# Optimization experiments

Hardware: AMD Instinct MI355X
Metric: run time of the kernel (lower is better)

The kernel has to match this reference:

```python
import jax, jax.numpy as jnp
import numpy as np

N = 50000      # nodes
E = 800000     # edges
H = 4          # attention heads
C = 64         # per-head channels (channel_in = channel_out = 64)
DIN = 128      # raw node feature dim (lazy Linear infers this)
D1 = H * C     # 256 = channel_in*4 concat dim
EPS = 1e-16    # PyG softmax eps
LN_EPS = 1e-5


def setup_inputs() -> dict:
    key = jax.random.key(0)
    ks = jax.random.split(key, 20)
    p = lambda k, shape: jax.random.normal(k, shape, jnp.float32) * 0.05
    return {
        "x": jax.random.normal(ks[0], (N, DIN), jnp.float32),
        "edge_index": jax.random.randint(ks[1], (2, E), 0, N, jnp.int32),
        # conv1 (GATConv with separate src/dst transforms, bipartite lazy mode)
        "Wsrc1": p(ks[2], (DIN, D1)), "Wdst1": p(ks[3], (DIN, D1)),
        "atts1": p(ks[4], (H, C)), "attd1": p(ks[5], (H, C)), "b1": p(ks[6], (D1,)),
        # lin1 skip
        "Wlin1": p(ks[7], (DIN, D1)), "blin1": p(ks[8], (D1,)),
        # LayerNorm
        "gamma": jnp.ones((D1,), jnp.float32), "beta": jnp.zeros((D1,), jnp.float32),
        # conv2
        "Wsrc2": p(ks[9], (D1, D1)), "Wdst2": p(ks[10], (D1, D1)),
        "atts2": p(ks[11], (H, C)), "attd2": p(ks[12], (H, C)), "b2": p(ks[13], (D1,)),
        # lin2 skip
        "Wlin2": p(ks[14], (D1, D1)), "blin2": p(ks[15], (D1,)),
    }


def gat_conv(x, src, dst, Wsrc, Wdst, atts, attd, bias):
    """PyG GATConv: gather -> leaky_relu score -> segment softmax over dst -> scatter-add."""
    n = x.shape[0]
    xs = (x @ Wsrc).reshape(n, H, C)   # source-side transform
    xd = (x @ Wdst).reshape(n, H, C)   # destination-side transform
    a_s = jnp.sum(xs * atts, axis=-1)  # [N,H]
    a_d = jnp.sum(xd * attd, axis=-1)  # [N,H]
    e = jax.nn.leaky_relu(a_s[src] + a_d[dst], 0.2)          # [E,H]
    m = jax.ops.segment_max(e, dst, num_segments=n)           # [N,H]
    m = jnp.where(jnp.isfinite(m), m, 0.0)                    # nodes with no in-edges
    ex = jnp.exp(e - m[dst])
    den = jax.ops.segment_sum(ex, dst, num_segments=n)
    alpha = ex / (den[dst] + EPS)                             # [E,H]
    out = jax.ops.segment_sum(xs[src] * alpha[:, :, None], dst, num_segments=n)
    return out.reshape(n, H * C) + bias                       # concat heads + bias


def reference(x, edge_index, Wsrc1, Wdst1, atts1, attd1, b1, Wlin1, blin1,
              gamma, beta, Wsrc2, Wdst2, atts2, attd2, b2, Wlin2, blin2):
    src, dst = edge_index[0], edge_index[1]
    h = gat_conv(x, src, dst, Wsrc1, Wdst1, atts1, attd1, b1) + x @ Wlin1 + blin1
    mu = jnp.mean(h, axis=-1, keepdims=True)
    var = jnp.mean((h - mu) ** 2, axis=-1, keepdims=True)
    h = (h - mu) * jax.lax.rsqrt(var + LN_EPS) * gamma + beta
    h = jax.nn.relu(h)
    out = gat_conv(h, src, dst, Wsrc2, Wdst2, atts2, attd2, b2) + h @ Wlin2 + blin2
    return out
```

## Files before the change

kernel.cpp:

```cpp
#include <hip/hip_runtime.h>
#include <float.h>

constexpr int DIN = 128;
constexpr int D1  = 256;
constexpr int HH  = 4;
constexpr int CC  = 64;

typedef _Float16 f16;
typedef __attribute__((ext_vector_type(2))) _Float16 f16x2;
typedef __attribute__((ext_vector_type(4))) _Float16 f16x4;
typedef __attribute__((ext_vector_type(8))) _Float16 f16x8;
typedef __attribute__((ext_vector_type(2))) float f32x2;
typedef __attribute__((ext_vector_type(4))) float f32x4;
typedef unsigned char u8;

#if __has_builtin(__builtin_amdgcn_cvt_pk_f32_fp8) && __has_builtin(__builtin_amdgcn_cvt_pk_fp8_f32)
#define HAS_CVT_FP8 1
#else
#define HAS_CVT_FP8 0
#include <hip/hip_fp8.h>
#endif

__device__ __forceinline__ u8 f2fp8(float f) {
#if HAS_CVT_FP8
    return (u8)(__builtin_amdgcn_cvt_pk_fp8_f32(f, f, 0, false) & 0xff);
#else
    __hip_fp8_e4m3 t(f);
    return (u8)t.__x;
#endif
}

__device__ __forceinline__ void fp8fma(unsigned w, float a, float4& acc) {
#if HAS_CVT_FP8
    f32x2 lo = __builtin_amdgcn_cvt_pk_f32_fp8((int)w, false);
    f32x2 hi = __builtin_amdgcn_cvt_pk_f32_fp8((int)w, true);
    acc.x = fmaf(lo[0], a, acc.x);
    acc.y = fmaf(lo[1], a, acc.y);
    acc.z = fmaf(hi[0], a, acc.z);
    acc.w = fmaf(hi[1], a, acc.w);
#else
    __hip_fp8_e4m3 b0, b1, b2, b3;
    b0.__x = (w) & 0xff; b1.__x = (w >> 8) & 0xff;
    b2.__x = (w >> 16) & 0xff; b3.__x = (w >> 24) & 0xff;
    acc.x = fmaf((float)b0, a, acc.x);
    acc.y = fmaf((float)b1, a, acc.y);
    acc.z = fmaf((float)b2, a, acc.z);
    acc.w = fmaf((float)b3, a, acc.w);
#endif
}

__device__ __forceinline__ float wave_sum(float v) {
    #pragma unroll
    for (int off = 32; off > 0; off >>= 1) v += __shfl_down(v, off, 64);
    return v;
}

__global__ __launch_bounds__(256) void pack_w_all_kernel(
        const float* __restrict__ Wsrc1, const float* __restrict__ Wlin1,
        const float* __restrict__ Wsrc2, const float* __restrict__ Wlin2,
        f16* __restrict__ WpS1, f16* __restrict__ WpL1,
        f16* __restrict__ WpS2, f16* __restrict__ WpL2) {
    int idx = blockIdx.x * 256 + threadIdx.x;
    const float *Wa, *Wb;
    f16 *Wpa, *Wpb;
    if (idx < DIN * D1) { Wa = Wsrc1; Wb = Wlin1; Wpa = WpS1; Wpb = WpL1; }
    else {
        idx -= DIN * D1;
        if (idx >= D1 * D1) return;
        Wa = Wsrc2; Wb = Wlin2; Wpa = WpS2; Wpb = WpL2;
    }
    int j    = idx & 7;
    int lane = (idx >> 3) & 63;
    int t    = idx >> 9;
    int ct   = t & 15, kt = t >> 4;
    int k    = kt * 32 + (lane >> 4) * 8 + j;
    int col  = ct * 16 + (lane & 15);
    size_t widx = (size_t)k * D1 + col;
    Wpa[idx] = (f16)Wa[widx];
    Wpb[idx] = (f16)Wb[widx];
}

__global__ __launch_bounds__(512) void make_v_all_kernel(
        const float* __restrict__ Wsrc1, const float* __restrict__ Wdst1,
        const float* __restrict__ atts1, const float* __restrict__ attd1,
        const float* __restrict__ Wsrc2, const float* __restrict__ Wdst2,
        const float* __restrict__ atts2, const float* __restrict__ attd2,
        float* __restrict__ Vs1, float* __restrict__ Vd1,
        float* __restrict__ Vs2, float* __restrict__ Vd2) {
    int kb = blockIdx.x;
    int w = threadIdx.x >> 6, lane = threadIdx.x & 63;
    int mat = w >> 2, h = w & 3;
    const float *W, *att;
    float* V;
    int k;
    if (kb < DIN) {
        k = kb;
        W = mat ? Wdst1 : Wsrc1; att = mat ? attd1 : atts1; V = mat ? Vd1 : Vs1;
    } else {
        k = kb - DIN;
        W = mat ? Wdst2 : Wsrc2; att = mat ? attd2 : atts2; V = mat ? Vd2 : Vs2;
    }
    float v = W[(size_t)k * D1 + h * CC + lane] * att[h * CC + lane];
    v = wave_sum(v);
    if (lane == 0) V[k * HH + h] = v;
}

__global__ __launch_bounds__(256) void cvt_scores_kernel(
        const float* __restrict__ X, const float* __restrict__ Vs,
        const float* __restrict__ Vd, f16* __restrict__ X16,
        float* __restrict__ a_s, float* __restrict__ a_d, int n) {
    constexpr int K = DIN, C = 32, SH = 5;
    __shared__ float4 VsL[K + 4];
    __shared__ float4 VdL[K + 4];
    for (int k = threadIdx.x; k < K; k += 256) {
        int ki = k + (k >> SH);
        VsL[ki] = reinterpret_cast<const float4*>(Vs)[k];
        VdL[ki] = reinterpret_cast<const float4*>(Vd)[k];
    }
    __syncthreads();

    const int lane  = threadIdx.x & 63;
    const int wid   = threadIdx.x >> 6;
    const int node  = blockIdx.x * 64 + wid * 16 + (lane >> 2);
    const int chunk = lane & 3;
    const int nodec = min(node, n - 1);
    const float* xp = X + (size_t)nodec * K + chunk * C;

    float xv[C];
    #pragma unroll
    for (int b = 0; b < C / 4; ++b) {
        float4 v = reinterpret_cast<const float4*>(xp)[b];
        xv[b * 4 + 0] = v.x; xv[b * 4 + 1] = v.y;
        xv[b * 4 + 2] = v.z; xv[b * 4 + 3] = v.w;
    }
    if (node < n) {
        f16* op = X16 + (size_t)node * K + chunk * C;
        #pragma unroll
        for (int b = 0; b < C / 8; ++b) {
            f16x8 o;
            #pragma unroll
            for (int t = 0; t < 8; ++t) o[t] = (f16)xv[b * 8 + t];
            reinterpret_cast<f16x8*>(op)[b] = o;
        }
    }

    float ps0 = 0.f, ps1 = 0.f, ps2 = 0.f, ps3 = 0.f;
    float pd0 = 0.f, pd1 = 0.f, pd2 = 0.f, pd3 = 0.f;
    #pragma unroll
    for (int t = 0; t < C; ++t) {
        int k  = chunk * C + t;
        int ki = k + (k >> SH);
        float xf = xv[t];
        float4 vs = VsL[ki];
        float4 vd = VdL[ki];
        ps0 = fmaf(xf, vs.x, ps0); ps1 = fmaf(xf, vs.y, ps1);
        ps2 = fmaf(xf, vs.z, ps2); ps3 = fmaf(xf, vs.w, ps3);
        pd0 = fmaf(xf, vd.x, pd0); pd1 = fmaf(xf, vd.y, pd1);
        pd2 = fmaf(xf, vd.z, pd2); pd3 = fmaf(xf, vd.w, pd3);
    }
    #pragma unroll
    for (int off = 1; off <= 2; off <<= 1) {
        ps0 += __shfl_xor(ps0, off, 64); ps1 += __shfl_xor(ps1, off, 64);
        ps2 += __shfl_xor(ps2, off, 64); ps3 += __shfl_xor(ps3, off, 64);
        pd0 += __shfl_xor(pd0, off, 64); pd1 += __shfl_xor(pd1, off, 64);
        pd2 += __shfl_xor(pd2, off, 64); pd3 += __shfl_xor(pd3, off, 64);
    }
    if (node < n) {
        float psv = chunk == 0 ? ps0 : chunk == 1 ? ps1 : chunk == 2 ? ps2 : ps3;
        float pdv = chunk == 0 ? pd0 : chunk == 1 ? pd1 : chunk == 2 ? pd2 : pd3;
        a_s[node * 4 + chunk] = psv;
        a_d[node * 4 + chunk] = pdv;
    }
}

__global__ __launch_bounds__(256) void deg_kernel(
        const int* __restrict__ dst, int* __restrict__ deg, int ne) {
    int e = blockIdx.x * 256 + threadIdx.x;
    if (e < ne) atomicAdd(deg + dst[e], 1);
}

__global__ __launch_bounds__(1024) void scan_phase1(
        const int* __restrict__ deg, int* __restrict__ partial,
        int* __restrict__ blocksum, int n) {
    __shared__ int tmp[1024];
    const int tid = threadIdx.x;
    int i = blockIdx.x * 1024 + tid;
    int v = (i < n) ? deg[i] : 0;
    tmp[tid] = v;
    __syncthreads();
    #pragma unroll
    for (int off = 1; off < 1024; off <<= 1) {
        int t = (tid >= off) ? tmp[tid - off] : 0;
        __syncthreads();
        tmp[tid] += t;
        __syncthreads();
    }
    if (i < n) partial[i] = tmp[tid];
    if (tid == 1023) blocksum[blockIdx.x] = tmp[1023];
}

__global__ __launch_bounds__(64) void scan_phase2(int* __restrict__ bs, int nb) {
    int lane = threadIdx.x;
    if (nb <= 64) {
        int v = (lane < nb) ? bs[lane] : 0;
        #pragma unroll
        for (int off = 1; off < 64; off <<= 1) {
            int t = __shfl_up(v, off, 64);
            if (lane >= off) v += t;
        }
        if (lane < nb) bs[lane] = v;
    } else if (lane == 0) {
        int acc = 0;
        for (int i = 0; i < nb; ++i) { acc += bs[i]; bs[i] = acc; }
    }
}

__global__ __launch_bounds__(1024) void scan_phase3(
        const int* __restrict__ partial, const int* __restrict__ bs,
        const int* __restrict__ deg, int* __restrict__ rowptr,
        int* __restrict__ degcur, int n) {
    int i = blockIdx.x * 1024 + threadIdx.x;
    if (i >= n) return;
    int add  = blockIdx.x ? bs[blockIdx.x - 1] : 0;
    int incl = partial[i] + add;
    rowptr[i + 1] = incl;
    degcur[i] = incl - deg[i];
    if (i == 0) rowptr[0] = 0;
}

__global__ __launch_bounds__(256) void fill_kernel(
        const int* __restrict__ src, const int* __restrict__ dst,
        int* __restrict__ cursor, int* __restrict__ srcs_csr, int ne) {
    int e = blockIdx.x * 256 + threadIdx.x;
    if (e >= ne) return;
    int pos = atomicAdd(cursor + dst[e], 1);
    srcs_csr[pos] = src[e];
}

template <int K>
__global__ __launch_bounds__(256) void gemm_dual_mfma(
        const f16* __restrict__ A, const f16* __restrict__ Wp1,
        const f16* __restrict__ Wp2, const float* __restrict__ bias1,
        const float* __restrict__ bias2, u8* __restrict__ O1,
        f16* __restrict__ O2, int n) {
    constexpr int KT = K / 32;
    const int lane = threadIdx.x & 63;
    const int w    = threadIdx.x >> 6;
    const int row0 = blockIdx.x * 64;
    const int col0 = w * 64;

    f32x4 acc1[4][4], acc2[4][4];
    const f32x4 zero = {0.f, 0.f, 0.f, 0.f};
    #pragma unroll
    for (int i = 0; i < 4; ++i)
        #pragma unroll
        for (int j = 0; j < 4; ++j) { acc1[i][j] = zero; acc2[i][j] = zero; }

    const f16* Arow[4];
    #pragma unroll
    for (int rf = 0; rf < 4; ++rf) {
        int ar = min(row0 + rf * 16 + (lane & 15), n - 1);
        Arow[rf] = A + (size_t)ar * K + (lane >> 4) * 8;
    }
    const f16* Wb1 = Wp1 + ((size_t)(w * 4) * 64 + lane) * 8;
    const f16* Wb2 = Wp2 + ((size_t)(w * 4) * 64 + lane) * 8;

    #pragma unroll
    for (int kt = 0; kt < KT; ++kt) {
        f16x8 a[4];
        #pragma unroll
        for (int rf = 0; rf < 4; ++rf)
            a[rf] = *reinterpret_cast<const f16x8*>(Arow[rf] + kt * 32);
        #pragma unroll
        for (int cf = 0; cf < 4; ++cf) {
            f16x8 b1v = *reinterpret_cast<const f16x8*>(Wb1 + (size_t)(kt * 16 + cf) * 512);
            f16x8 b2v = *reinterpret_cast<const f16x8*>(Wb2 + (size_t)(kt * 16 + cf) * 512);
            #pragma unroll
            for (int rf = 0; rf < 4; ++rf) {
                acc1[rf][cf] = __builtin_amdgcn_mfma_f32_16x16x32_f16(a[rf], b1v, acc1[rf][cf], 0, 0, 0);
                acc2[rf][cf] = __builtin_amdgcn_mfma_f32_16x16x32_f16(a[rf], b2v, acc2[rf][cf], 0, 0, 0);
            }
        }
    }

    #pragma unroll
    for (int cf = 0; cf < 4; ++cf) {
        const int col = col0 + cf * 16 + (lane & 15);
        const float bsum = bias1[col] + bias2[col];
        #pragma unroll
        for (int rf = 0; rf < 4; ++rf) {
            #pragma unroll
            for (int r = 0; r < 4; ++r) {
                const int row = row0 + rf * 16 + (lane >> 4) * 4 + r;
                if (row < n) {
                    O1[(size_t)row * D1 + col] = f2fp8(acc1[rf][cf][r]);
                    O2[(size_t)row * D1 + col] = (f16)(acc2[rf][cf][r] + bsum);
                }
            }
        }
    }
}

#define ALDS_STRIDE 66

__device__ __forceinline__ float4 gat_node_acc(
        const int* __restrict__ srcs, const float* __restrict__ a_s,
        const u8* __restrict__ xs, f16* __restrict__ alds,
        const float* __restrict__ a_d_row, int base, int deg, int lane) {
    const int h = lane >> 4;
    const int j = lane & 15;
    const float adv = a_d_row[h];
    float den = 0.f;
    float4 acc = {0.f, 0.f, 0.f, 0.f};
    const f16* arow = alds + h * ALDS_STRIDE;

    for (int c0 = 0; c0 < deg; c0 += 16) {
        const int cnt = min(16, deg - c0);
        const int idx = c0 + j;
        const bool valid = idx < deg;
        const int sl = srcs[base + min(idx, deg - 1)];
        {
            float e = a_s[(size_t)sl * 4 + h] + adv;
            e = e > 0.f ? e : 0.2f * e;
            float a = valid ? __expf(e) : 0.f;
            den += a;
            alds[h * ALDS_STRIDE + j] = (f16)a;
        }
        asm volatile("s_waitcnt lgkmcnt(0)" ::: "memory");

        const int sv = sl;
        for (int i = 0; i < cnt; i += 4) {
            int s1 = __shfl(sv, i, 64);
            int s2 = __shfl(sv, i + 1, 64);
            int s3 = __shfl(sv, i + 2, 64);
            int s4 = __shfl(sv, i + 3, 64);
            f16x2 alA = *reinterpret_cast<const f16x2*>(arow + i);
            f16x2 alB = *reinterpret_cast<const f16x2*>(arow + i + 2);
            unsigned x1 = *reinterpret_cast<const unsigned*>(xs + (size_t)s1 * D1 + lane * 4);
            unsigned x2 = *reinterpret_cast<const unsigned*>(xs + (size_t)s2 * D1 + lane * 4);
            unsigned x3 = *reinterpret_cast<const unsigned*>(xs + (size_t)s3 * D1 + lane * 4);
            unsigned x4 = *reinterpret_cast<const unsigned*>(xs + (size_t)s4 * D1 + lane * 4);
            fp8fma(x1, (float)alA.x, acc);
            fp8fma(x2, (float)alA.y, acc);
            fp8fma(x3, (float)alB.x, acc);
            fp8fma(x4, (float)alB.y, acc);
        }
    }

    #pragma unroll
    for (int off = 1; off < 16; off <<= 1)
        den += __shfl_xor(den, off, 64);
    const float invd = 1.f / (den + 1e-16f);
    acc.x *= invd; acc.y *= invd; acc.z *= invd; acc.w *= invd;
    return acc;
}

__global__ __launch_bounds__(256) void gat_gather_ln_kernel(
        const int* __restrict__ rowptr, const int* __restrict__ srcs,
        const float* __restrict__ a_s1, const float* __restrict__ a_d1,
        const u8* __restrict__ xs, const f16* __restrict__ skip,
        const float* __restrict__ gamma, const float* __restrict__ beta,
        const float* __restrict__ Vs2, const float* __restrict__ Vd2,
        f16* __restrict__ hout, float* __restrict__ a_s2,
        float* __restrict__ a_d2, int n) {
    __shared__ f16 alpha_lds[4][4 * ALDS_STRIDE];
    const int wid = threadIdx.x >> 6, lane = threadIdx.x & 63;
    const int d = blockIdx.x * 4 + wid;
    if (d >= n) return;
    const int base = rowptr[d];
    const int deg  = rowptr[d + 1] - base;

    float4 acc = {0.f, 0.f, 0.f, 0.f};
    if (deg > 0)
        acc = gat_node_acc(srcs, a_s1, xs, alpha_lds[wid],
                           a_d1 + (size_t)d * 4, base, deg, lane);

    f16x4 sk = *reinterpret_cast<const f16x4*>(skip + (size_t)d * D1 + lane * 4);
    float4 v;
    v.x = acc.x + (float)sk[0];
    v.y = acc.y + (float)sk[1];
    v.z = acc.z + (float)sk[2];
    v.w = acc.w + (float)sk[3];

    float s  = v.x + v.y + v.z + v.w;
    float sq = v.x * v.x + v.y * v.y + v.z * v.z + v.w * v.w;
    #pragma unroll
    for (int off = 32; off > 0; off >>= 1) {
        s  += __shfl_down(s, off, 64);
        sq += __shfl_down(sq, off, 64);
    }
    s  = __shfl(s, 0, 64);
    sq = __shfl(sq, 0, 64);
    float mu  = s * (1.f / 256.f);
    float var = sq * (1.f / 256.f) - mu * mu;
    float rstd = rsqrtf(var + 1e-5f);
    float4 g = *reinterpret_cast<const float4*>(gamma + lane * 4);
    float4 b = *reinterpret_cast<const float4*>(beta + lane * 4);
    f16x4 o;
    o[0] = (f16)fmaxf((v.x - mu) * rstd * g.x + b.x, 0.f);
    o[1] = (f16)fmaxf((v.y - mu) * rstd * g.y + b.y, 0.f);
    o[2] = (f16)fmaxf((v.z - mu) * rstd * g.z + b.z, 0.f);
    o[3] = (f16)fmaxf((v.w - mu) * rstd * g.w + b.w, 0.f);
    *reinterpret_cast<f16x4*>(hout + (size_t)d * D1 + lane * 4) = o;

    float of0 = (float)o[0], of1 = (float)o[1], of2 = (float)o[2], of3 = (float)o[3];
    const float4* V4s = reinterpret_cast<const float4*>(Vs2);
    const float4* V4d = reinterpret_cast<const float4*>(Vd2);
    float4 r0 = V4s[lane * 4 + 0], r1 = V4s[lane * 4 + 1];
    float4 r2 = V4s[lane * 4 + 2], r3 = V4s[lane * 4 + 3];
    float4 ps;
    ps.x = of0 * r0.x + of1 * r1.x + of2 * r2.x + of3 * r3.x;
    ps.y = of0 * r0.y + of1 * r1.y + of2 * r2.y + of3 * r3.y;
    ps.z = of0 * r0.z + of1 * r1.z + of2 * r2.z + of3 * r3.z;
    ps.w = of0 * r0.w + of1 * r1.w + of2 * r2.w + of3 * r3.w;
    r0 = V4d[lane * 4 + 0]; r1 = V4d[lane * 4 + 1];
    r2 = V4d[lane * 4 + 2]; r3 = V4d[lane * 4 + 3];
    float4 pd;
    pd.x = of0 * r0.x + of1 * r1.x + of2 * r2.x + of3 * r3.x;
    pd.y = of0 * r0.y + of1 * r1.y + of2 * r2.y + of3 * r3.y;
    pd.z = of0 * r0.z + of1 * r1.z + of2 * r2.z + of3 * r3.z;
    pd.w = of0 * r0.w + of1 * r1.w + of2 * r2.w + of3 * r3.w;
    #pragma unroll
    for (int off = 1; off < 64; off <<= 1) {
        ps.x += __shfl_xor(ps.x, off, 64); ps.y += __shfl_xor(ps.y, off, 64);
        ps.z += __shfl_xor(ps.z, off, 64); ps.w += __shfl_xor(ps.w, off, 64);
        pd.x += __shfl_xor(pd.x, off, 64); pd.y += __shfl_xor(pd.y, off, 64);
        pd.z += __shfl_xor(pd.z, off, 64); pd.w += __shfl_xor(pd.w, off, 64);
    }
    if (lane == 0) {
        *reinterpret_cast<float4*>(a_s2 + (size_t)d * 4) = ps;
        *reinterpret_cast<float4*>(a_d2 + (size_t)d * 4) = pd;
    }
}

__global__ __launch_bounds__(256) void gat_gather_out_kernel(
        const int* __restrict__ rowptr, const int* __restrict__ srcs,
        const float* __restrict__ a_s, const float* __restrict__ a_d,
        const u8* __restrict__ xs, const f16* __restrict__ skip2,
        float* __restrict__ out, int n) {
    __shared__ f16 alpha_lds[4][4 * ALDS_STRIDE];
    const int wid = threadIdx.x >> 6, lane = threadIdx.x & 63;
    const int d = blockIdx.x * 4 + wid;
    if (d >= n) return;
    const int base = rowptr[d];
    const int deg  = rowptr[d + 1] - base;
    float4 acc = {0.f, 0.f, 0.f, 0.f};
    if (deg > 0)
        acc = gat_node_acc(srcs, a_s, xs, alpha_lds[wid],
                           a_d + (size_t)d * 4, base, deg, lane);
    f16x4 sk = *reinterpret_cast<const f16x4*>(skip2 + (size_t)d * D1 + lane * 4);
    float4 ov;
    ov.x = acc.x + (float)sk[0];
    ov.y = acc.y + (float)sk[1];
    ov.z = acc.z + (float)sk[2];
    ov.w = acc.w + (float)sk[3];
    *reinterpret_cast<float4*>(out + (size_t)d * D1 + lane * 4) = ov;
}

extern "C" void kernel_launch(void* const* d_in, const int* in_sizes, int n_in,
                              void* d_out, int out_size, void* d_ws, size_t ws_size,
                              hipStream_t stream) {
    const float* x     = (const float*)d_in[0];
    const int*   ei    = (const int*)d_in[1];
    const float* Wsrc1 = (const float*)d_in[2];
    const float* Wdst1 = (const float*)d_in[3];
    const float* atts1 = (const float*)d_in[4];
    const float* attd1 = (const float*)d_in[5];
    const float* b1    = (const float*)d_in[6];
    const float* Wlin1 = (const float*)d_in[7];
    const float* blin1 = (const float*)d_in[8];
    const float* gamma = (const float*)d_in[9];
    const float* beta  = (const float*)d_in[10];
    const float* Wsrc2 = (const float*)d_in[11];
    const float* Wdst2 = (const float*)d_in[12];
    const float* atts2 = (const float*)d_in[13];
    const float* attd2 = (const float*)d_in[14];
    const float* b2    = (const float*)d_in[15];
    const float* Wlin2 = (const float*)d_in[16];
    const float* blin2 = (const float*)d_in[17];

    const int n  = in_sizes[0] / DIN;
    const int ne = in_sizes[1] / 2;
    const int* src = ei;
    const int* dst = ei + ne;

    char* w8 = (char*)d_ws;
    size_t off = 0;
    auto alloc = [&](size_t bytes) -> void* {
        void* p = w8 + off;
        off += (bytes + 255) & ~(size_t)255;
        return p;
    };
    f16*  h16    = (f16*)alloc((size_t)n * D1 * 2);
    f16*  x16    = h16;
    u8*   xs8    = (u8*)alloc((size_t)n * D1);
    f16*  skip1  = (f16*)alloc((size_t)n * D1 * 2);
    float* a_s1  = (float*)alloc((size_t)n * HH * 4);
    float* a_d1  = (float*)alloc((size_t)n * HH * 4);
    float* a_s2  = (float*)alloc((size_t)n * HH * 4);
    float* a_d2  = (float*)alloc((size_t)n * HH * 4);
    float* Vs1   = (float*)alloc((size_t)D1 * HH * 4);
    float* Vd1   = (float*)alloc((size_t)D1 * HH * 4);
    float* Vs2   = (float*)alloc((size_t)D1 * HH * 4);
    float* Vd2   = (float*)alloc((size_t)D1 * HH * 4);
    int* rowptr   = (int*)alloc(((size_t)n + 1) * 4);
    int* degbuf   = (int*)alloc((size_t)n * 4);
    int* degcur   = (int*)alloc((size_t)n * 4);
    int* partial  = (int*)alloc((size_t)n * 4);
    int* blocksum = (int*)alloc(1024 * 4);
    int* srcs_csr = (int*)alloc((size_t)ne * 4);
    f16* WpS1  = (f16*)alloc((size_t)DIN * D1 * 2);
    f16* WpL1  = (f16*)alloc((size_t)DIN * D1 * 2);
    f16* WpS2  = (f16*)alloc((size_t)D1 * D1 * 2);
    f16* WpL2  = (f16*)alloc((size_t)D1 * D1 * 2);

    float* out = (float*)d_out;

    const int nb_node4  = (n + 3) / 4;
    const int nb_node64 = (n + 63) / 64;
    const int nb_e      = (ne + 255) / 256;
    const int nb_gemm   = (n + 63) / 64;
    const int nb_scan   = (n + 1023) / 1024;
    const int nb_pack   = (DIN * D1 + D1 * D1 + 255) / 256;

    (void)hipMemsetAsync(degbuf, 0, (size_t)n * 4, stream);
    deg_kernel<<<nb_e, 256, 0, stream>>>(dst, degbuf, ne);
    scan_phase1<<<nb_scan, 1024, 0, stream>>>(degbuf, partial, blocksum, n);
    scan_phase2<<<1, 64, 0, stream>>>(blocksum, nb_scan);
    scan_phase3<<<nb_scan, 1024, 0, stream>>>(partial, blocksum, degbuf, rowptr, degcur, n);
    fill_kernel<<<nb_e, 256, 0, stream>>>(src, dst, degcur, srcs_csr, ne);
    pack_w_all_kernel<<<nb_pack, 256, 0, stream>>>(Wsrc1, Wlin1, Wsrc2, Wlin2,
                                                   WpS1, WpL1, WpS2, WpL2);
    make_v_all_kernel<<<DIN + D1, 512, 0, stream>>>(Wsrc1, Wdst1, atts1, attd1,
                                                    Wsrc2, Wdst2, atts2, attd2,
                                                    Vs1, Vd1, Vs2, Vd2);

    cvt_scores_kernel<<<nb_node64, 256, 0, stream>>>(x, Vs1, Vd1, x16, a_s1, a_d1, n);
    gemm_dual_mfma<DIN><<<nb_gemm, 256, 0, stream>>>(x16, WpS1, WpL1, b1, blin1, xs8, skip1, n);
    gat_gather_ln_kernel<<<nb_node4, 256, 0, stream>>>(rowptr, srcs_csr, a_s1, a_d1, xs8,
                                                       skip1, gamma, beta, Vs2, Vd2,
                                                       h16, a_s2, a_d2, n);

    gemm_dual_mfma<D1><<<nb_gemm, 256, 0, stream>>>(h16, WpS2, WpL2, b2, blin2, xs8, skip1, n);
    gat_gather_out_kernel<<<nb_node4, 256, 0, stream>>>(rowptr, srcs_csr, a_s2, a_d2,
                                                        xs8, skip1, out, n);
}
```

Measured before the change: 286.4 us.

## Merge prep kernels, fold scan phase2, widen fp8 gathers, cheaper score reduction

Merges the weight packing and attention-vector kernels into one launch. The separate block-sum scan kernel is removed, and each scan_phase3 block now sums the preceding block sums itself. The GAT gather loop now loads 8 fp8 bytes per lane, so each lane covers two edges in parallel across the two wave halves, and the halves are recombined with shuffles. The final per-node score reduction is replaced by a transpose-style butterfly that uses fewer shuffles. The goal is to cut launch count, gather load instructions and shuffle traffic, at the cost of extra shuffles after the gather loop. The inline scan only works when there are at most 64 scan blocks.

```diff
diff --git a/kernel.cpp b/kernel.cpp
--- a/kernel.cpp
+++ b/kernel.cpp
@@ -55,54 +55,54 @@
     return v;
 }
 
-__global__ __launch_bounds__(256) void pack_w_all_kernel(
+__global__ __launch_bounds__(256) void prep_w_kernel(
         const float* __restrict__ Wsrc1, const float* __restrict__ Wlin1,
         const float* __restrict__ Wsrc2, const float* __restrict__ Wlin2,
+        const float* __restrict__ Wdst1, const float* __restrict__ Wdst2,
+        const float* __restrict__ atts1, const float* __restrict__ attd1,
+        const float* __restrict__ atts2, const float* __restrict__ attd2,
         f16* __restrict__ WpS1, f16* __restrict__ WpL1,
-        f16* __restrict__ WpS2, f16* __restrict__ WpL2) {
-    int idx = blockIdx.x * 256 + threadIdx.x;
-    const float *Wa, *Wb;
-    f16 *Wpa, *Wpb;
-    if (idx < DIN * D1) { Wa = Wsrc1; Wb = Wlin1; Wpa = WpS1; Wpb = WpL1; }
-    else {
-        idx -= DIN * D1;
-        if (idx >= D1 * D1) return;
-        Wa = Wsrc2; Wb = Wlin2; Wpa = WpS2; Wpb = WpL2;
-    }
-    int j    = idx & 7;
-    int lane = (idx >> 3) & 63;
-    int t    = idx >> 9;
-    int ct   = t & 15, kt = t >> 4;
-    int k    = kt * 32 + (lane >> 4) * 8 + j;
-    int col  = ct * 16 + (lane & 15);
-    size_t widx = (size_t)k * D1 + col;
-    Wpa[idx] = (f16)Wa[widx];
-    Wpb[idx] = (f16)Wb[widx];
-}
-
-__global__ __launch_bounds__(512) void make_v_all_kernel(
-        const float* __restrict__ Wsrc1, const float* __restrict__ Wdst1,
-        const float* __restrict__ atts1, const float* __restrict__ attd1,
-        const float* __restrict__ Wsrc2, const float* __restrict__ Wdst2,
-        const float* __restrict__ atts2, const float* __restrict__ attd2,
+        f16* __restrict__ WpS2, f16* __restrict__ WpL2,
         float* __restrict__ Vs1, float* __restrict__ Vd1,
-        float* __restrict__ Vs2, float* __restrict__ Vd2) {
-    int kb = blockIdx.x;
-    int w = threadIdx.x >> 6, lane = threadIdx.x & 63;
-    int mat = w >> 2, h = w & 3;
-    const float *W, *att;
-    float* V;
-    int k;
-    if (kb < DIN) {
-        k = kb;
-        W = mat ? Wdst1 : Wsrc1; att = mat ? attd1 : atts1; V = mat ? Vd1 : Vs1;
+        float* __restrict__ Vs2, float* __restrict__ Vd2, int nb_pack) {
+    if ((int)blockIdx.x < nb_pack) {
+        int idx = blockIdx.x * 256 + threadIdx.x;
+        const float *Wa, *Wb;
+        f16 *Wpa, *Wpb;
+        if (idx < DIN * D1) { Wa = Wsrc1; Wb = Wlin1; Wpa = WpS1; Wpb = WpL1; }
+        else {
+            idx -= DIN * D1;
+            if (idx >= D1 * D1) return;
+            Wa = Wsrc2; Wb = Wlin2; Wpa = WpS2; Wpb = WpL2;
+        }
+        int j    = idx & 7;
+        int lane = (idx >> 3) & 63;
+        int t    = idx >> 9;
+        int ct   = t & 15, kt = t >> 4;
+        int k    = kt * 32 + (lane >> 4) * 8 + j;
+        int col  = ct * 16 + (lane & 15);
+        size_t widx = (size_t)k * D1 + col;
+        Wpa[idx] = (f16)Wa[widx];
+        Wpb[idx] = (f16)Wb[widx];
     } else {
-        k = kb - DIN;
-        W = mat ? Wdst2 : Wsrc2; att = mat ? attd2 : atts2; V = mat ? Vd2 : Vs2;
-    }
-    float v = W[(size_t)k * D1 + h * CC + lane] * att[h * CC + lane];
-    v = wave_sum(v);
-    if (lane == 0) V[k * HH + h] = v;
+        int b2  = blockIdx.x - nb_pack;
+        int mat = b2 & 1;
+        int kb  = b2 >> 1;
+        int h = threadIdx.x >> 6, lane = threadIdx.x & 63;
+        const float *W, *att;
+        float* V;
+        int k;
+        if (kb < DIN) {
+            k = kb;
+            W = mat ? Wdst1 : Wsrc1; att = mat ? attd1 : atts1; V = mat ? Vd1 : Vs1;
+        } else {
+            k = kb - DIN;
+            W = mat ? Wdst2 : Wsrc2; att = mat ? attd2 : atts2; V = mat ? Vd2 : Vs2;
+        }
+        float v = W[(size_t)k * D1 + h * CC + lane] * att[h * CC + lane];
+        v = wave_sum(v);
+        if (lane == 0) V[k * HH + h] = v;
+    }
 }
 
 __global__ __launch_bounds__(256) void cvt_scores_kernel(
@@ -199,29 +199,22 @@
     if (tid == 1023) blocksum[blockIdx.x] = tmp[1023];
 }
 
-__global__ __launch_bounds__(64) void scan_phase2(int* __restrict__ bs, int nb) {
-    int lane = threadIdx.x;
-    if (nb <= 64) {
-        int v = (lane < nb) ? bs[lane] : 0;
-        #pragma unroll
-        for (int off = 1; off < 64; off <<= 1) {
-            int t = __shfl_up(v, off, 64);
-            if (lane >= off) v += t;
-        }
-        if (lane < nb) bs[lane] = v;
-    } else if (lane == 0) {
-        int acc = 0;
-        for (int i = 0; i < nb; ++i) { acc += bs[i]; bs[i] = acc; }
-    }
-}
-
 __global__ __launch_bounds__(1024) void scan_phase3(
-        const int* __restrict__ partial, const int* __restrict__ bs,
+        const int* __restrict__ partial, const int* __restrict__ blocksum,
         const int* __restrict__ deg, int* __restrict__ rowptr,
         int* __restrict__ degcur, int n) {
+    __shared__ int add_s;
+    if (threadIdx.x < 64) {
+        int lane = threadIdx.x;
+        int v = (lane < (int)blockIdx.x) ? blocksum[lane] : 0;
+        #pragma unroll
+        for (int off = 32; off > 0; off >>= 1) v += __shfl_down(v, off, 64);
+        if (lane == 0) add_s = v;
+    }
+    __syncthreads();
+    const int add = add_s;
     int i = blockIdx.x * 1024 + threadIdx.x;
     if (i >= n) return;
-    int add  = blockIdx.x ? bs[blockIdx.x - 1] : 0;
     int incl = partial[i] + add;
     rowptr[i + 1] = incl;
     degcur[i] = incl - deg[i];
@@ -307,12 +300,15 @@
         const int* __restrict__ srcs, const float* __restrict__ a_s,
         const u8* __restrict__ xs, f16* __restrict__ alds,
         const float* __restrict__ a_d_row, int base, int deg, int lane) {
-    const int h = lane >> 4;
-    const int j = lane & 15;
+    const int h    = lane >> 4;
+    const int j    = lane & 15;
+    const int pair = lane >> 5;
+    const int ch32 = lane & 31;
+    const f16* arow_i = alds + (ch32 >> 3) * ALDS_STRIDE;
     const float adv = a_d_row[h];
     float den = 0.f;
-    float4 acc = {0.f, 0.f, 0.f, 0.f};
-    const f16* arow = alds + h * ALDS_STRIDE;
+    float4 accLo = {0.f, 0.f, 0.f, 0.f};
+    float4 accHi = {0.f, 0.f, 0.f, 0.f};
 
     for (int c0 = 0; c0 < deg; c0 += 16) {
         const int cnt = min(16, deg - c0);
@@ -330,22 +326,33 @@
 
         const int sv = sl;
         for (int i = 0; i < cnt; i += 4) {
-            int s1 = __shfl(sv, i, 64);
-            int s2 = __shfl(sv, i + 1, 64);
-            int s3 = __shfl(sv, i + 2, 64);
-            int s4 = __shfl(sv, i + 3, 64);
-            f16x2 alA = *reinterpret_cast<const f16x2*>(arow + i);
-            f16x2 alB = *reinterpret_cast<const f16x2*>(arow + i + 2);
-            unsigned x1 = *reinterpret_cast<const unsigned*>(xs + (size_t)s1 * D1 + lane * 4);
-            unsigned x2 = *reinterpret_cast<const unsigned*>(xs + (size_t)s2 * D1 + lane * 4);
-            unsigned x3 = *reinterpret_cast<const unsigned*>(xs + (size_t)s3 * D1 + lane * 4);
-            unsigned x4 = *reinterpret_cast<const unsigned*>(xs + (size_t)s4 * D1 + lane * 4);
-            fp8fma(x1, (float)alA.x, acc);
-            fp8fma(x2, (float)alA.y, acc);
-            fp8fma(x3, (float)alB.x, acc);
-            fp8fma(x4, (float)alB.y, acc);
-        }
-    }
+            int sA = __shfl(sv, i + pair, 64);
+            int sB = __shfl(sv, i + 2 + pair, 64);
+            float aA = (float)arow_i[i + pair];
+            float aB = (float)arow_i[i + 2 + pair];
+            uint2 xA = *reinterpret_cast<const uint2*>(xs + (size_t)sA * D1 + ch32 * 8);
+            uint2 xB = *reinterpret_cast<const uint2*>(xs + (size_t)sB * D1 + ch32 * 8);
+            fp8fma(xA.x, aA, accLo);
+            fp8fma(xA.y, aA, accHi);
+            fp8fma(xB.x, aB, accLo);
+            fp8fma(xB.y, aB, accHi);
+        }
+    }
+
+    accLo.x += __shfl_xor(accLo.x, 32, 64); accLo.y += __shfl_xor(accLo.y, 32, 64);
+    accLo.z += __shfl_xor(accLo.z, 32, 64); accLo.w += __shfl_xor(accLo.w, 32, 64);
+    accHi.x += __shfl_xor(accHi.x, 32, 64); accHi.y += __shfl_xor(accHi.y, 32, 64);
+    accHi.z += __shfl_xor(accHi.z, 32, 64); accHi.w += __shfl_xor(accHi.w, 32, 64);
+
+    const int srcl = lane >> 1;
+    float l0 = __shfl(accLo.x, srcl, 64), l1 = __shfl(accLo.y, srcl, 64);
+    float l2 = __shfl(accLo.z, srcl, 64), l3 = __shfl(accLo.w, srcl, 64);
+    float h0 = __shfl(accHi.x, srcl, 64), h1 = __shfl(accHi.y, srcl, 64);
+    float h2 = __shfl(accHi.z, srcl, 64), h3 = __shfl(accHi.w, srcl, 64);
+    const bool hi = (lane & 1) != 0;
+    float4 acc;
+    acc.x = hi ? h0 : l0; acc.y = hi ? h1 : l1;
+    acc.z = hi ? h2 : l2; acc.w = hi ? h3 : l3;
 
     #pragma unroll
     for (int off = 1; off < 16; off <<= 1)
@@ -408,28 +415,34 @@
     const float4* V4d = reinterpret_cast<const float4*>(Vd2);
     float4 r0 = V4s[lane * 4 + 0], r1 = V4s[lane * 4 + 1];
     float4 r2 = V4s[lane * 4 + 2], r3 = V4s[lane * 4 + 3];
-    float4 ps;
-    ps.x = of0 * r0.x + of1 * r1.x + of2 * r2.x + of3 * r3.x;
-    ps.y = of0 * r0.y + of1 * r1.y + of2 * r2.y + of3 * r3.y;
-    ps.z = of0 * r0.z + of1 * r1.z + of2 * r2.z + of3 * r3.z;
-    ps.w = of0 * r0.w + of1 * r1.w + of2 * r2.w + of3 * r3.w;
+    float v0 = of0 * r0.x + of1 * r1.x + of2 * r2.x + of3 * r3.x;
+    float v1 = of0 * r0.y + of1 * r1.y + of2 * r2.y + of3 * r3.y;
+    float v2 = of0 * r0.z + of1 * r1.z + of2 * r2.z + of3 * r3.z;
+    float v3 = of0 * r0.w + of1 * r1.w + of2 * r2.w + of3 * r3.w;
     r0 = V4d[lane * 4 + 0]; r1 = V4d[lane * 4 + 1];
     r2 = V4d[lane * 4 + 2]; r3 = V4d[lane * 4 + 3];
-    float4 pd;
-    pd.x = of0 * r0.x + of1 * r1.x + of2 * r2.x + of3 * r3.x;
-    pd.y = of0 * r0.y + of1 * r1.y + of2 * r2.y + of3 * r3.y;
-    pd.z = of0 * r0.z + of1 * r1.z + of2 * r2.z + of3 * r3.z;
-    pd.w = of0 * r0.w + of1 * r1.w + of2 * r2.w + of3 * r3.w;
-    #pragma unroll
-    for (int off = 1; off < 64; off <<= 1) {
-        ps.x += __shfl_xor(ps.x, off, 64); ps.y += __shfl_xor(ps.y, off, 64);
-        ps.z += __shfl_xor(ps.z, off, 64); ps.w += __shfl_xor(ps.w, off, 64);
-        pd.x += __shfl_xor(pd.x, off, 64); pd.y += __shfl_xor(pd.y, off, 64);
-        pd.z += __shfl_xor(pd.z, off, 64); pd.w += __shfl_xor(pd.w, off, 64);
-    }
-    if (lane == 0) {
-        *reinterpret_cast<float4*>(a_s2 + (size_t)d * 4) = ps;
-        *reinterpret_cast<float4*>(a_d2 + (size_t)d * 4) = pd;
+    float v4 = of0 * r0.x + of1 * r1.x + of2 * r2.x + of3 * r3.x;
+    float v5 = of0 * r0.y + of1 * r1.y + of2 * r2.y + of3 * r3.y;
+    float v6 = of0 * r0.z + of1 * r1.z + of2 * r2.z + of3 * r3.z;
+    float v7 = of0 * r0.w + of1 * r1.w + of2 * r2.w + of3 * r3.w;
+
+    const bool b0 = (lane & 1) != 0;
+    float w0 = (b0 ? v1 : v0) + __shfl_xor(b0 ? v0 : v1, 1, 64);
+    float w1 = (b0 ? v3 : v2) + __shfl_xor(b0 ? v2 : v3, 1, 64);
+    float w2 = (b0 ? v5 : v4) + __shfl_xor(b0 ? v4 : v5, 1, 64);
+    float w3 = (b0 ? v7 : v6) + __shfl_xor(b0 ? v6 : v7, 1, 64);
+    const bool b1 = (lane & 2) != 0;
+    float u0 = (b1 ? w1 : w0) + __shfl_xor(b1 ? w0 : w1, 2, 64);
+    float u1 = (b1 ? w3 : w2) + __shfl_xor(b1 ? w2 : w3, 2, 64);
+    const bool b2f = (lane & 4) != 0;
+    float z = (b2f ? u1 : u0) + __shfl_xor(b2f ? u0 : u1, 4, 64);
+    z += __shfl_xor(z, 8, 64);
+    z += __shfl_xor(z, 16, 64);
+    z += __shfl_xor(z, 32, 64);
+    if (lane < 8) {
+        float* outp = (lane < 4) ? (a_s2 + (size_t)d * 4 + lane)
+                                 : (a_d2 + (size_t)d * 4 + (lane - 4));
+        *outp = z;
     }
 }
 
@@ -526,14 +539,12 @@
     (void)hipMemsetAsync(degbuf, 0, (size_t)n * 4, stream);
     deg_kernel<<<nb_e, 256, 0, stream>>>(dst, degbuf, ne);
     scan_phase1<<<nb_scan, 1024, 0, stream>>>(degbuf, partial, blocksum, n);
-    scan_phase2<<<1, 64, 0, stream>>>(blocksum, nb_scan);
     scan_phase3<<<nb_scan, 1024, 0, stream>>>(partial, blocksum, degbuf, rowptr, degcur, n);
     fill_kernel<<<nb_e, 256, 0, stream>>>(src, dst, degcur, srcs_csr, ne);
-    pack_w_all_kernel<<<nb_pack, 256, 0, stream>>>(Wsrc1, Wlin1, Wsrc2, Wlin2,
-                                                   WpS1, WpL1, WpS2, WpL2);
-    make_v_all_kernel<<<DIN + D1, 512, 0, stream>>>(Wsrc1, Wdst1, atts1, attd1,
-                                                    Wsrc2, Wdst2, atts2, attd2,
-                                                    Vs1, Vd1, Vs2, Vd2);
+    prep_w_kernel<<<nb_pack + 2 * (DIN + D1), 256, 0, stream>>>(
+        Wsrc1, Wlin1, Wsrc2, Wlin2, Wdst1, Wdst2,
+        atts1, attd1, atts2, attd2,
+        WpS1, WpL1, WpS2, WpL2, Vs1, Vd1, Vs2, Vd2, nb_pack);
 
     cvt_scores_kernel<<<nb_node64, 256, 0, stream>>>(x, Vs1, Vd1, x16, a_s1, a_d1, n);
     gemm_dual_mfma<DIN><<<nb_gemm, 256, 0, stream>>>(x16, WpS1, WpL1, b1, blin1, xs8, skip1, n);
```

New measurement: 289.4 us. About the same (+1.1%).
